# Kernel optimization log

Hardware: AMD Instinct MI355X
Metric: run time of the kernel (lower is better)

The kernel has to match this reference:

```python
import jax, jax.numpy as jnp
import numpy as np

LN_EPS = 1e-5


def setup_inputs() -> dict:
    key = jax.random.key(0)
    k1, = jax.random.split(key, 1)
    B, C, H, W = 16, 512, 64, 64
    HW = H * W
    x = jax.random.normal(k1, (B, C, H, W), dtype=jnp.float32)
    gamma = jnp.ones((), dtype=jnp.float32)          # Scale(1) learnable scalar
    ln_weight = jnp.ones((HW,), dtype=jnp.float32)   # LayerNorm weight
    ln_bias = jnp.zeros((HW,), dtype=jnp.float32)    # LayerNorm bias
    return {"x": x, "gamma": gamma, "ln_weight": ln_weight, "ln_bias": ln_bias}


def reference(x, gamma, ln_weight, ln_bias):
    B, C, H, W = x.shape
    v = x.reshape(B, C, H * W)                       # [B, C, HW] (Q = K = V)
    energy = jnp.einsum('bcn,bdn->bcd', v, v)        # [B, C, C]
    attn = jax.nn.softmax(energy, axis=-1)
    out = jnp.einsum('bcd,bdn->bcn', attn, v)        # [B, C, HW]
    out = gamma * out + v                            # scale + residual
    # LayerNorm over last dim (HW), torch eps=1e-5
    mean = jnp.mean(out, axis=-1, keepdims=True)
    var = jnp.mean(jnp.square(out - mean), axis=-1, keepdims=True)
    out = (out - mean) * jax.lax.rsqrt(var + LN_EPS) * ln_weight + ln_bias
    return out.reshape(B, C, H, W)
```

## Files before the change

### kernel.cpp

```cpp
#include <hip/hip_runtime.h>
#include <hip/hip_bf16.h>

#define B_DIM 16
#define C_DIM 512
#define HW_DIM 4096
#define LN_EPS 1e-5f

using bf16 = __hip_bfloat16;
typedef __bf16 v8bf __attribute__((ext_vector_type(8)));
typedef float v4f __attribute__((ext_vector_type(4)));
typedef unsigned short v8us __attribute__((ext_vector_type(8)));
using gptr_t = const __attribute__((address_space(1))) void*;
using lptr_t = __attribute__((address_space(3))) void*;

__device__ __forceinline__ unsigned short f2bf(float f) {
  unsigned int u = __float_as_uint(f);
  u = (u + 0x7fffu + ((u >> 16) & 1u)) >> 16;
  return (unsigned short)u;
}
__device__ __forceinline__ float bf2f(unsigned short us) {
  return __uint_as_float(((unsigned int)us) << 16);
}

__global__ __launch_bounds__(256) void k_convert_transpose(
    const float* __restrict__ x, unsigned short* __restrict__ v,
    unsigned short* __restrict__ vt) {
  __shared__ unsigned short tile[64][66];
  const int tid = threadIdx.x;
  const int b = blockIdx.z;
  const int n0 = blockIdx.x * 64;
  const int c0 = blockIdx.y * 64;
  const size_t boff = (size_t)b * ((size_t)C_DIM * HW_DIM);
  const float* xb = x + boff;
  unsigned short* vb = v + boff;
  unsigned short* vtb = vt + boff;

  const int cl = tid >> 3;
  const int h8 = (tid & 7) * 8;
#pragma unroll
  for (int j = 0; j < 2; ++j) {
    const int c = cl + j * 32;
    const float* src = xb + (size_t)(c0 + c) * HW_DIM + n0 + h8;
    const float4 f0 = ((const float4*)src)[0];
    const float4 f1 = ((const float4*)src)[1];
    v8us pack;
    pack[0] = f2bf(f0.x); pack[1] = f2bf(f0.y);
    pack[2] = f2bf(f0.z); pack[3] = f2bf(f0.w);
    pack[4] = f2bf(f1.x); pack[5] = f2bf(f1.y);
    pack[6] = f2bf(f1.z); pack[7] = f2bf(f1.w);
    *(v8us*)(vb + (size_t)(c0 + c) * HW_DIM + n0 + h8) = pack;
#pragma unroll
    for (int e = 0; e < 8; ++e) tile[c][h8 + e] = pack[e];
  }
  __syncthreads();
  const int nl = tid >> 3;
  const int c8 = (tid & 7) * 8;
#pragma unroll
  for (int j = 0; j < 2; ++j) {
    const int n = nl + j * 32;
    v8us pack;
#pragma unroll
    for (int e = 0; e < 8; ++e) pack[e] = tile[c8 + e][n];
    *(v8us*)(vtb + (size_t)(n0 + n) * C_DIM + c0 + c8) = pack;
  }
}

__device__ __forceinline__ void stage_tiles(
    const bf16* __restrict__ a_base, const bf16* __restrict__ b_base,
    const int stride, const int k0, const int wave, const int lane,
    bf16* ldsA, bf16* ldsB) {
  const int srow = lane >> 3;
  const int skcol = (lane & 7) * 8;
#pragma unroll
  for (int i = 0; i < 4; ++i) {
    const int ci = wave * 4 + i;
    const int row = ci * 8 + srow;
    __builtin_amdgcn_global_load_lds(
        (gptr_t)(a_base + (size_t)row * stride + k0 + skcol),
        (lptr_t)(ldsA + ci * 512), 16, 0, 0);
    __builtin_amdgcn_global_load_lds(
        (gptr_t)(b_base + (size_t)row * stride + k0 + skcol),
        (lptr_t)(ldsB + ci * 512), 16, 0, 0);
  }
}

__device__ __forceinline__ void compute_tile(
    const bf16* ldsA, const bf16* ldsB, const int wave, const int lane,
    v4f acc[4][4]) {
  const int kb = (lane >> 4) * 8;
  const int rl = lane & 15;
  const int wr = wave >> 1, wc = wave & 1;
#pragma unroll
  for (int kk = 0; kk < 2; ++kk) {
    v8bf af[4], bfr[4];
#pragma unroll
    for (int m = 0; m < 4; ++m)
      af[m] = *(const v8bf*)(ldsA + (wr * 64 + m * 16 + rl) * 64 + kk * 32 + kb);
#pragma unroll
    for (int n = 0; n < 4; ++n)
      bfr[n] = *(const v8bf*)(ldsB + (wc * 64 + n * 16 + rl) * 64 + kk * 32 + kb);
#pragma unroll
    for (int m = 0; m < 4; ++m)
#pragma unroll
      for (int n = 0; n < 4; ++n)
        acc[m][n] = __builtin_amdgcn_mfma_f32_16x16x32_bf16(af[m], bfr[n], acc[m][n], 0, 0, 0);
  }
}

__device__ __forceinline__ void gemm_dbuf_loop(
    const bf16* __restrict__ a_base, const bf16* __restrict__ b_base,
    const int stride, const int ksteps, const int wave, const int lane,
    bf16* ldsA0, bf16* ldsB0, bf16* ldsA1, bf16* ldsB1, v4f acc[4][4]) {
  stage_tiles(a_base, b_base, stride, 0, wave, lane, ldsA0, ldsB0);
  __syncthreads();
  int cur = 0;
  for (int kt = 0; kt < ksteps - 1; ++kt) {
    if (cur == 0)
      stage_tiles(a_base, b_base, stride, (kt + 1) * 64, wave, lane, ldsA1, ldsB1);
    else
      stage_tiles(a_base, b_base, stride, (kt + 1) * 64, wave, lane, ldsA0, ldsB0);
    compute_tile(cur == 0 ? ldsA0 : ldsA1, cur == 0 ? ldsB0 : ldsB1, wave, lane, acc);
    __syncthreads();
    cur ^= 1;
  }
  compute_tile(cur == 0 ? ldsA0 : ldsA1, cur == 0 ? ldsB0 : ldsB1, wave, lane, acc);
}

__global__ __launch_bounds__(256) void k_gemm1(
    const bf16* __restrict__ v, float* __restrict__ e_part) {
  __shared__ __align__(16) bf16 lds[4][128 * 64];
  int t = blockIdx.x;
  const int ks = t >> 8;
  t &= 255;
  const int b = t >> 4;
  const int cb = (t >> 2) & 3;
  const int db = t & 3;
  const int tid = threadIdx.x;
  const int wave = tid >> 6, lane = tid & 63;
  const bf16* vb = v + (size_t)b * ((size_t)C_DIM * HW_DIM) + ks * (HW_DIM / 2);
  v4f acc[4][4] = {};
  gemm_dbuf_loop(vb + (size_t)(cb * 128) * HW_DIM,
                 vb + (size_t)(db * 128) * HW_DIM,
                 HW_DIM, (HW_DIM / 2) / 64, wave, lane,
                 lds[0], lds[1], lds[2], lds[3], acc);
  float* eb = e_part + (size_t)ks * ((size_t)B_DIM * C_DIM * C_DIM) +
              (size_t)b * (C_DIM * C_DIM);
  const int wr = wave >> 1, wc = wave & 1;
  const int rl = lane & 15;
  const int r0 = (lane >> 4) * 4;
#pragma unroll
  for (int m = 0; m < 4; ++m)
#pragma unroll
    for (int n = 0; n < 4; ++n) {
      const int row0 = cb * 128 + wr * 64 + m * 16 + r0;
      const int col = db * 128 + wc * 64 + n * 16 + rl;
#pragma unroll
      for (int r = 0; r < 4; ++r)
        eb[(size_t)(row0 + r) * C_DIM + col] = acc[m][n][r];
    }
}

__global__ __launch_bounds__(256) void k_softmax(
    const float* __restrict__ e_part, unsigned short* __restrict__ attn) {
  const int row = blockIdx.x;
  const float* e0 = e_part + (size_t)row * C_DIM;
  const float* e1 = e0 + (size_t)B_DIM * C_DIM * C_DIM;
  const int tid = threadIdx.x;
  const float v0 = e0[tid] + e1[tid];
  const float v1 = e0[tid + 256] + e1[tid + 256];
  float mx = fmaxf(v0, v1);
#pragma unroll
  for (int off = 32; off > 0; off >>= 1) mx = fmaxf(mx, __shfl_xor(mx, off));
  __shared__ float rmax[4], rsum[4];
  const int wv = tid >> 6, ln = tid & 63;
  if (ln == 0) rmax[wv] = mx;
  __syncthreads();
  mx = fmaxf(fmaxf(rmax[0], rmax[1]), fmaxf(rmax[2], rmax[3]));
  const float p0 = __expf(v0 - mx), p1 = __expf(v1 - mx);
  float s = p0 + p1;
#pragma unroll
  for (int off = 32; off > 0; off >>= 1) s += __shfl_xor(s, off);
  if (ln == 0) rsum[wv] = s;
  __syncthreads();
  s = rsum[0] + rsum[1] + rsum[2] + rsum[3];
  const float inv = 1.0f / s;
  attn[(size_t)row * C_DIM + tid] = f2bf(p0 * inv);
  attn[(size_t)row * C_DIM + tid + 256] = f2bf(p1 * inv);
}

__global__ __launch_bounds__(256) void k_gemm2(
    const bf16* __restrict__ attn, const bf16* __restrict__ vt,
    const unsigned short* __restrict__ vres, const float* __restrict__ gamma,
    float* __restrict__ out) {
  __shared__ __align__(16) bf16 lds[4][128 * 64];
  const int bidx = blockIdx.x;
  const int b = bidx >> 7;
  const int cb = (bidx >> 5) & 3;
  const int nb = bidx & 31;
  const int tid = threadIdx.x;
  const int wave = tid >> 6, lane = tid & 63;
  const bf16* ab = attn + (size_t)b * (C_DIM * C_DIM) + (size_t)(cb * 128) * C_DIM;
  const bf16* bb = vt + (size_t)b * ((size_t)C_DIM * HW_DIM) + (size_t)(nb * 128) * C_DIM;
  v4f acc[4][4] = {};
  gemm_dbuf_loop(ab, bb, C_DIM, C_DIM / 64, wave, lane,
                 lds[0], lds[1], lds[2], lds[3], acc);
  const float g = gamma[0];
  const size_t boff = (size_t)b * ((size_t)C_DIM * HW_DIM);
  const unsigned short* xb = vres + boff;
  float* ob = out + boff;
  const int wr = wave >> 1, wc = wave & 1;
  const int rl = lane & 15;
  const int r0 = (lane >> 4) * 4;
#pragma unroll
  for (int m = 0; m < 4; ++m)
#pragma unroll
    for (int n = 0; n < 4; ++n) {
      const int c0 = cb * 128 + wr * 64 + m * 16 + r0;
      const int nn = nb * 128 + wc * 64 + n * 16 + rl;
#pragma unroll
      for (int r = 0; r < 4; ++r) {
        const size_t idx = (size_t)(c0 + r) * HW_DIM + nn;
        ob[idx] = g * acc[m][n][r] + bf2f(xb[idx]);
      }
    }
}

__global__ __launch_bounds__(256) void k_ln(
    float* __restrict__ out, const float* __restrict__ w,
    const float* __restrict__ bias) {
  const int row = blockIdx.x;
  float* p = out + (size_t)row * HW_DIM;
  const int tid = threadIdx.x;
  float4 vals[4];
  float s = 0.f, ss = 0.f;
#pragma unroll
  for (int i = 0; i < 4; ++i) {
    const float4 vv = ((const float4*)p)[tid + i * 256];
    vals[i] = vv;
    s += vv.x + vv.y + vv.z + vv.w;
    ss += vv.x * vv.x + vv.y * vv.y + vv.z * vv.z + vv.w * vv.w;
  }
#pragma unroll
  for (int off = 32; off > 0; off >>= 1) {
    s += __shfl_xor(s, off);
    ss += __shfl_xor(ss, off);
  }
  __shared__ float rs[4], rss[4];
  const int wv = tid >> 6, ln = tid & 63;
  if (ln == 0) { rs[wv] = s; rss[wv] = ss; }
  __syncthreads();
  s = rs[0] + rs[1] + rs[2] + rs[3];
  ss = rss[0] + rss[1] + rss[2] + rss[3];
  const float mean = s * (1.f / HW_DIM);
  const float var = ss * (1.f / HW_DIM) - mean * mean;
  const float rstd = rsqrtf(var + LN_EPS);
#pragma unroll
  for (int i = 0; i < 4; ++i) {
    const int idx = tid + i * 256;
    const float4 vv = vals[i];
    const float4 w4 = ((const float4*)w)[idx];
    const float4 b4 = ((const float4*)bias)[idx];
    float4 r;
    r.x = (vv.x - mean) * rstd * w4.x + b4.x;
    r.y = (vv.y - mean) * rstd * w4.y + b4.y;
    r.z = (vv.z - mean) * rstd * w4.z + b4.z;
    r.w = (vv.w - mean) * rstd * w4.w + b4.w;
    ((float4*)p)[idx] = r;
  }
}

extern "C" void kernel_launch(void* const* d_in, const int* in_sizes, int n_in,
                              void* d_out, int out_size, void* d_ws, size_t ws_size,
                              hipStream_t stream) {
  const float* x = (const float*)d_in[0];
  const float* gamma = (const float*)d_in[1];
  const float* lnw = (const float*)d_in[2];
  const float* lnb = (const float*)d_in[3];
  float* out = (float*)d_out;
  char* ws = (char*)d_ws;

  const size_t n_elem = (size_t)B_DIM * C_DIM * HW_DIM;
  const size_t e_elems = (size_t)B_DIM * C_DIM * C_DIM;
  unsigned short* vbf = (unsigned short*)ws;
  unsigned short* vbfT = (unsigned short*)(ws + 2 * n_elem);
  float* e_part = (float*)(ws + 4 * n_elem);
  unsigned short* attn =
      (unsigned short*)(ws + 4 * n_elem + 2 * e_elems * sizeof(float));

  k_convert_transpose<<<dim3(HW_DIM / 64, C_DIM / 64, B_DIM), 256, 0, stream>>>(
      x, vbf, vbfT);
  k_gemm1<<<512, 256, 0, stream>>>((const bf16*)vbf, e_part);
  k_softmax<<<B_DIM * C_DIM, 256, 0, stream>>>(e_part, attn);
  k_gemm2<<<B_DIM * 128, 256, 0, stream>>>((const bf16*)attn, (const bf16*)vbfT,
                                           vbf, gamma, out);
  k_ln<<<B_DIM * C_DIM, 256, 0, stream>>>(out, lnw, lnb);
}
```

Baseline: 245.2 us.

## Rewrite gemm2 with 256x256 tiles, 8 waves, and interleaved staging schedule

Replaces the 128x128 gemm2 tile with a 256x256 tile computed by 8 waves (512 threads), using XOR-swizzled LDS staging via global_load_lds and a hand-scheduled loop that interleaves fragment loads, MFMA phases with setprio, and next-tile prefetch. The block index is remapped so that consecutive blocks spread across batches/XCDs. The goal is more operand reuse per LDS load and better latency hiding. In exchange it raises register pressure and relies on fragile manual waitcnt and barrier ordering.

```diff
diff --git a/kernel.cpp b/kernel.cpp
--- a/kernel.cpp
+++ b/kernel.cpp
@@ -188,39 +188,154 @@
   attn[(size_t)row * C_DIM + tid + 256] = f2bf(p1 * inv);
 }
 
-__global__ __launch_bounds__(256) void k_gemm2(
+#define TILE_E (256 * 64)
+
+__device__ __forceinline__ void stage_half8(
+    const bf16* __restrict__ g, bf16* l, int k0, int wave, int lane) {
+  const int lrow = lane >> 3, lc = lane & 7;
+#pragma unroll
+  for (int i = 0; i < 2; ++i) {
+    const int row = i * 64 + wave * 8 + lrow;
+    __builtin_amdgcn_global_load_lds(
+        (gptr_t)(g + (size_t)row * C_DIM + k0 + ((lc ^ (row & 7)) << 3)),
+        (lptr_t)(l + (i * 64 + wave * 8) * 64), 16, 0, 0);
+  }
+}
+__device__ __forceinline__ void stage_op2(
+    const bf16* __restrict__ g, bf16* l, int k0, int wave, int lane) {
+  stage_half8(g, l, k0, wave, lane);
+  stage_half8(g + (size_t)128 * C_DIM, l + 128 * 64, k0, wave, lane);
+}
+__device__ __forceinline__ v8bf ld_frag8(const bf16* l, int row, int j) {
+  return *(const v8bf*)(l + row * 64 + ((j ^ (row & 7)) << 3));
+}
+
+__global__ __launch_bounds__(512, 2) void k_gemm2(
     const bf16* __restrict__ attn, const bf16* __restrict__ vt,
     const unsigned short* __restrict__ vres, const float* __restrict__ gamma,
     float* __restrict__ out) {
-  __shared__ __align__(16) bf16 lds[4][128 * 64];
-  const int bidx = blockIdx.x;
-  const int b = bidx >> 7;
-  const int cb = (bidx >> 5) & 3;
-  const int nb = bidx & 31;
+  __shared__ __align__(16) bf16 smA[2][TILE_E];
+  __shared__ __align__(16) bf16 smB[2][TILE_E];
+  const int bid = blockIdx.x;
+  const int t = (bid & 7) * 64 + (bid >> 3);
+  const int b = t >> 5;
+  const int cb = (t >> 4) & 1;
+  const int nb = t & 15;
   const int tid = threadIdx.x;
   const int wave = tid >> 6, lane = tid & 63;
-  const bf16* ab = attn + (size_t)b * (C_DIM * C_DIM) + (size_t)(cb * 128) * C_DIM;
-  const bf16* bb = vt + (size_t)b * ((size_t)C_DIM * HW_DIM) + (size_t)(nb * 128) * C_DIM;
-  v4f acc[4][4] = {};
-  gemm_dbuf_loop(ab, bb, C_DIM, C_DIM / 64, wave, lane,
-                 lds[0], lds[1], lds[2], lds[3], acc);
+  const int wm = wave >> 2, wn = wave & 3;
+  const int rl = lane & 15, kq = lane >> 4;
+
+  const bf16* Ab = attn + (size_t)b * (C_DIM * C_DIM) + (size_t)(cb * 256) * C_DIM;
+  const bf16* Bb = vt + (size_t)b * ((size_t)C_DIM * HW_DIM) + (size_t)(nb * 256) * C_DIM;
+
+  v4f acc[8][4] = {};
+
+  stage_op2(Bb, smB[0], 0, wave, lane);
+  stage_op2(Ab, smA[0], 0, wave, lane);
+  stage_op2(Bb, smB[1], 64, wave, lane);
+  stage_op2(Ab, smA[1], 64, wave, lane);
+  asm volatile("s_waitcnt vmcnt(8)" ::: "memory");
+  __builtin_amdgcn_s_barrier();
+
+  v8bf a[4][2], b01[2][2], b23[2][2];
+  for (int kt = 0; kt < 8; ++kt) {
+    const bf16* LA = smA[kt & 1];
+    const bf16* LB = smB[kt & 1];
+#pragma unroll
+    for (int mi = 0; mi < 4; ++mi)
+#pragma unroll
+      for (int kk = 0; kk < 2; ++kk)
+        a[mi][kk] = ld_frag8(LA, wm * 128 + mi * 16 + rl, kk * 4 + kq);
+#pragma unroll
+    for (int ni = 0; ni < 2; ++ni)
+#pragma unroll
+      for (int kk = 0; kk < 2; ++kk)
+        b01[ni][kk] = ld_frag8(LB, wn * 64 + ni * 16 + rl, kk * 4 + kq);
+    __builtin_amdgcn_s_barrier();
+    asm volatile("s_waitcnt lgkmcnt(0)");
+    __builtin_amdgcn_s_setprio(1);
+#pragma unroll
+    for (int kk = 0; kk < 2; ++kk)
+#pragma unroll
+      for (int mi = 0; mi < 4; ++mi)
+#pragma unroll
+        for (int ni = 0; ni < 2; ++ni)
+          acc[mi][ni] = __builtin_amdgcn_mfma_f32_16x16x32_bf16(
+              a[mi][kk], b01[ni][kk], acc[mi][ni], 0, 0, 0);
+    __builtin_amdgcn_s_setprio(0);
+    __builtin_amdgcn_s_barrier();
+#pragma unroll
+    for (int ni = 0; ni < 2; ++ni)
+#pragma unroll
+      for (int kk = 0; kk < 2; ++kk)
+        b23[ni][kk] = ld_frag8(LB, wn * 64 + (ni + 2) * 16 + rl, kk * 4 + kq);
+    __builtin_amdgcn_s_barrier();
+    asm volatile("s_waitcnt lgkmcnt(0)");
+    __builtin_amdgcn_s_setprio(1);
+#pragma unroll
+    for (int kk = 0; kk < 2; ++kk)
+#pragma unroll
+      for (int mi = 0; mi < 4; ++mi)
+#pragma unroll
+        for (int ni = 0; ni < 2; ++ni)
+          acc[mi][ni + 2] = __builtin_amdgcn_mfma_f32_16x16x32_bf16(
+              a[mi][kk], b23[ni][kk], acc[mi][ni + 2], 0, 0, 0);
+    __builtin_amdgcn_s_setprio(0);
+    __builtin_amdgcn_s_barrier();
+#pragma unroll
+    for (int mi = 0; mi < 4; ++mi)
+#pragma unroll
+      for (int kk = 0; kk < 2; ++kk)
+        a[mi][kk] = ld_frag8(LA, wm * 128 + (mi + 4) * 16 + rl, kk * 4 + kq);
+    if (kt < 6) stage_op2(Bb, smB[kt & 1], (kt + 2) * 64, wave, lane);
+    __builtin_amdgcn_s_barrier();
+    asm volatile("s_waitcnt lgkmcnt(0)");
+    __builtin_amdgcn_s_setprio(1);
+#pragma unroll
+    for (int kk = 0; kk < 2; ++kk)
+#pragma unroll
+      for (int mi = 0; mi < 4; ++mi)
+#pragma unroll
+        for (int ni = 0; ni < 2; ++ni)
+          acc[mi + 4][ni + 2] = __builtin_amdgcn_mfma_f32_16x16x32_bf16(
+              a[mi][kk], b23[ni][kk], acc[mi + 4][ni + 2], 0, 0, 0);
+    __builtin_amdgcn_s_setprio(0);
+    __builtin_amdgcn_s_barrier();
+    if (kt < 6) stage_op2(Ab, smA[kt & 1], (kt + 2) * 64, wave, lane);
+    __builtin_amdgcn_s_barrier();
+    __builtin_amdgcn_s_setprio(1);
+#pragma unroll
+    for (int kk = 0; kk < 2; ++kk)
+#pragma unroll
+      for (int mi = 0; mi < 4; ++mi)
+#pragma unroll
+        for (int ni = 0; ni < 2; ++ni)
+          acc[mi + 4][ni] = __builtin_amdgcn_mfma_f32_16x16x32_bf16(
+              a[mi][kk], b01[ni][kk], acc[mi + 4][ni], 0, 0, 0);
+    __builtin_amdgcn_s_setprio(0);
+    if (kt < 6)
+      asm volatile("s_waitcnt vmcnt(8)" ::: "memory");
+    else if (kt == 6)
+      asm volatile("s_waitcnt vmcnt(0)" ::: "memory");
+    __builtin_amdgcn_s_barrier();
+  }
+
   const float g = gamma[0];
   const size_t boff = (size_t)b * ((size_t)C_DIM * HW_DIM);
   const unsigned short* xb = vres + boff;
   float* ob = out + boff;
-  const int wr = wave >> 1, wc = wave & 1;
-  const int rl = lane & 15;
-  const int r0 = (lane >> 4) * 4;
-#pragma unroll
-  for (int m = 0; m < 4; ++m)
-#pragma unroll
-    for (int n = 0; n < 4; ++n) {
-      const int c0 = cb * 128 + wr * 64 + m * 16 + r0;
-      const int nn = nb * 128 + wc * 64 + n * 16 + rl;
+  const int r0 = kq * 4;
+#pragma unroll
+  for (int mi = 0; mi < 8; ++mi)
+#pragma unroll
+    for (int ni = 0; ni < 4; ++ni) {
+      const int c0 = cb * 256 + wm * 128 + mi * 16 + r0;
+      const int nn = nb * 256 + wn * 64 + ni * 16 + rl;
 #pragma unroll
       for (int r = 0; r < 4; ++r) {
         const size_t idx = (size_t)(c0 + r) * HW_DIM + nn;
-        ob[idx] = g * acc[m][n][r] + bf2f(xb[idx]);
+        ob[idx] = g * acc[mi][ni][r] + bf2f(xb[idx]);
       }
     }
 }
@@ -291,7 +406,7 @@
       x, vbf, vbfT);
   k_gemm1<<<512, 256, 0, stream>>>((const bf16*)vbf, e_part);
   k_softmax<<<B_DIM * C_DIM, 256, 0, stream>>>(e_part, attn);
-  k_gemm2<<<B_DIM * 128, 256, 0, stream>>>((const bf16*)attn, (const bf16*)vbfT,
-                                           vbf, gamma, out);
+  k_gemm2<<<512, 512, 0, stream>>>((const bf16*)attn, (const bf16*)vbfT,
+                                   vbf, gamma, out);
   k_ln<<<B_DIM * C_DIM, 256, 0, stream>>>(out, lnw, lnb);
 }
```

Measured after the change: 231.0 us. 5.8% less time.
